# Kernel optimization log

Hardware: AMD Instinct MI355X
Metric: run time of the kernel (lower is better)

The kernel has to match this reference:

```python
import jax, jax.numpy as jnp
import numpy as np

N, E, D_IN, D_OUT = 50000, 800000, 128, 128
LN_EPS = 1e-5


def setup_inputs() -> dict:
    key = jax.random.key(0)
    ks = jax.random.split(key, 7)
    x = jax.random.normal(ks[0], (N, D_IN), dtype=jnp.float32)
    adj = jax.random.randint(ks[1], (2, E), 0, N, dtype=jnp.int32)  # edge_index
    scale = 1.0 / np.sqrt(D_IN)
    W_gcn = jax.random.normal(ks[2], (D_IN, D_OUT), dtype=jnp.float32) * scale
    b_gcn = jax.random.normal(ks[3], (D_OUT,), dtype=jnp.float32) * 0.02
    W_lin = jax.random.normal(ks[4], (D_IN, D_OUT), dtype=jnp.float32) * scale
    ln_w = jnp.ones((D_OUT,), dtype=jnp.float32)
    ln_b = jnp.zeros((D_OUT,), dtype=jnp.float32)
    return {"adj": adj, "x": x, "W_gcn": W_gcn, "b_gcn": b_gcn,
            "W_lin": W_lin, "ln_w": ln_w, "ln_b": ln_b}


def _gcn_conv(x, edge_index, W, b):
    """PyG GCNConv: add self-loops, symmetric D^-1/2 (A+I) D^-1/2 normalization."""
    n = x.shape[0]
    loop = jnp.arange(n, dtype=edge_index.dtype)
    src = jnp.concatenate([edge_index[0], loop])  # message sources (x_j)
    dst = jnp.concatenate([edge_index[1], loop])  # aggregation targets
    ones = jnp.ones(src.shape[0], dtype=x.dtype)
    deg = jax.ops.segment_sum(ones, dst, num_segments=n)
    dinv = jnp.where(deg > 0, jax.lax.rsqrt(deg), 0.0)
    norm = dinv[src] * dinv[dst]                   # [E+N]
    h = x @ W                                      # [N, D_OUT] project first (PyG order)
    msg = h[src] * norm[:, None]                   # gather + scale
    agg = jax.ops.segment_sum(msg, dst, num_segments=n)
    return agg + b


def _layer_norm(y, w, b):
    mu = jnp.mean(y, axis=-1, keepdims=True)
    var = jnp.mean(jnp.square(y - mu), axis=-1, keepdims=True)
    return (y - mu) * jax.lax.rsqrt(var + LN_EPS) * w + b


def reference(adj, x, W_gcn, b_gcn, W_lin, ln_w, ln_b):
    x1 = _gcn_conv(x, adj, W_gcn, b_gcn)
    x2 = x @ W_lin                                  # bias=False linear
    return _layer_norm(x1 + x2 + 1e-6, ln_w, ln_b)
```

## Files before the change

kernel.cpp:

```cpp
#include <hip/hip_runtime.h>
#include <hip/hip_bf16.h>

#define NN 50000
#define EE 800000
#define DD 128
#define NB 196

typedef __attribute__((ext_vector_type(8))) short bf16x8;
typedef __attribute__((ext_vector_type(4))) float f32x4;

static __device__ __forceinline__ unsigned short f2bf(float f) {
  union { float f; unsigned u; } v; v.f = f;
  unsigned r = v.u + 0x7FFFu + ((v.u >> 16) & 1u);
  return (unsigned short)(r >> 16);
}
static __device__ __forceinline__ float bf2f(unsigned short h) {
  union { unsigned u; float f; } v; v.u = ((unsigned)h) << 16;
  return v.f;
}

__global__ __launch_bounds__(256) void k_p0(const int* __restrict__ dst,
                                            int* __restrict__ bucketCnt,
                                            const float* __restrict__ Wg,
                                            const float* __restrict__ Wl,
                                            unsigned short* __restrict__ Wt) {
  int b = blockIdx.x, t = threadIdx.x;
  if (b < NB) {
    __shared__ int cnt[NB];
    for (int i = t; i < NB; i += 256) cnt[i] = 0;
    __syncthreads();
    int e0 = b * 4096;
    for (int i = t; i < 4096; i += 256) {
      int e = e0 + i;
      if (e < EE) atomicAdd(&cnt[dst[e] >> 8], 1);
    }
    __syncthreads();
    for (int i = t; i < NB; i += 256)
      if (cnt[i]) atomicAdd(&bucketCnt[i], cnt[i]);
  } else {
    for (int i = (b - NB) * 256 + t; i < DD * 256; i += 32 * 256) {
      int n = i >> 8, k = i & 255;
      float v = (k < 128) ? Wg[k * DD + n] : Wl[(k - 128) * DD + n];
      Wt[i] = f2bf(v);
    }
  }
}

__global__ __launch_bounds__(256) void k_pscan(const int* __restrict__ bucketCnt,
                                               int* __restrict__ bucketStart,
                                               int* __restrict__ cursor) {
  __shared__ int s[256];
  int t = threadIdx.x;
  int v = (t < NB) ? bucketCnt[t] : 0;
  s[t] = v;
  for (int off = 1; off < 256; off <<= 1) {
    __syncthreads();
    int tmp = (t >= off) ? s[t - off] : 0;
    __syncthreads();
    if (t >= off) s[t] += tmp;
  }
  __syncthreads();
  if (t < NB) {
    int excl = s[t] - v;
    bucketStart[t] = excl;
    cursor[t] = excl;
  }
}

__global__ __launch_bounds__(256) void k_p1(const int* __restrict__ src,
                                            const int* __restrict__ dst,
                                            int* __restrict__ cursor,
                                            unsigned int* __restrict__ pairs) {
  __shared__ unsigned int stage[4096];
  __shared__ int cnt[NB], base[NB], cur[NB];
  int t = threadIdx.x;
  int e0 = blockIdx.x * 4096;
  for (int i = t; i < NB; i += 256) { cnt[i] = 0; cur[i] = 0; }
  __syncthreads();
  for (int i = t; i < 4096; i += 256) {
    int e = e0 + i;
    unsigned int p = 0xFFFFFFFFu;
    if (e < EE) {
      int d = dst[e];
      int s = src[e];
      int bk = d >> 8;
      p = (unsigned int)s | ((unsigned int)(d & 255) << 16) | ((unsigned int)bk << 24);
      atomicAdd(&cnt[bk], 1);
    }
    stage[i] = p;
  }
  __syncthreads();
  for (int i = t; i < NB; i += 256)
    base[i] = cnt[i] ? atomicAdd(&cursor[i], cnt[i]) : 0;
  __syncthreads();
  for (int i = t; i < 4096; i += 256) {
    unsigned int p = stage[i];
    if (p != 0xFFFFFFFFu) {
      int bk = p >> 24;
      int ofs = atomicAdd(&cur[bk], 1);
      pairs[base[bk] + ofs] = p;
    }
  }
}

__global__ __launch_bounds__(256) void k_p2(
    const unsigned int* __restrict__ pairs, const int* __restrict__ bucketStart,
    const int* __restrict__ bucketCnt, const float4* __restrict__ x4,
    int* __restrict__ deg, float* __restrict__ dinv, int* __restrict__ rowStart,
    int* __restrict__ srcList, ushort4* __restrict__ xs4,
    ushort4* __restrict__ axc4) {
  int b = blockIdx.x, t = threadIdx.x;
  __shared__ int ldeg[256], lscan[256], lcur[256];
  __shared__ float ldinv[256];
  int n0 = b << 8;
  int nloc = NN - n0; if (nloc > 256) nloc = 256;
  int start = bucketStart[b], cnt = bucketCnt[b];
  ldeg[t] = 0;
  __syncthreads();
  for (int i = t; i < cnt; i += 256)
    atomicAdd(&ldeg[(pairs[start + i] >> 16) & 255], 1);
  __syncthreads();
  int dg = ldeg[t];
  lscan[t] = dg;
  for (int off = 1; off < 256; off <<= 1) {
    __syncthreads();
    int tmp = (t >= off) ? lscan[t - off] : 0;
    __syncthreads();
    if (t >= off) lscan[t] += tmp;
  }
  __syncthreads();
  int rs = start + lscan[t] - dg;
  lcur[t] = rs;
  float di = rsqrtf((float)(dg + 1));
  ldinv[t] = di;
  if (t < nloc) {
    deg[n0 + t] = dg;
    dinv[n0 + t] = di;
    rowStart[n0 + t] = rs;
  }
  __syncthreads();
  for (int i = t; i < cnt; i += 256) {
    unsigned int p = pairs[start + i];
    int pos = atomicAdd(&lcur[(p >> 16) & 255], 1);
    srcList[pos] = (int)(p & 0xFFFFu);
  }
  for (int i = t; i < nloc * 32; i += 256) {
    int r = i >> 5, c4 = i & 31;
    float4 v = x4[(size_t)(n0 + r) * 32 + c4];
    float d = ldinv[r];
    ushort4 s, rw;
    s.x = f2bf(v.x * d); s.y = f2bf(v.y * d);
    s.z = f2bf(v.z * d); s.w = f2bf(v.w * d);
    rw.x = f2bf(v.x); rw.y = f2bf(v.y); rw.z = f2bf(v.z); rw.w = f2bf(v.w);
    xs4[(size_t)(n0 + r) * 32 + c4] = s;
    axc4[(size_t)(n0 + r) * 64 + 32 + c4] = rw;
  }
}

__global__ __launch_bounds__(256) void k_agg(
    const unsigned short* __restrict__ xs, const float* __restrict__ dinv,
    const int* __restrict__ rowStart, const int* __restrict__ deg,
    const int* __restrict__ srcList, unsigned short* __restrict__ axc) {
  int t = threadIdx.x;
  int w = t >> 6, lane = t & 63;
  int node = blockIdx.x * 4 + w;
  if (node >= NN) return;
  int g = lane >> 4, r = lane & 15;
  int c0 = r * 8;
  float acc[8];
#pragma unroll
  for (int i = 0; i < 8; i++) acc[i] = 0.f;
  if (g == 0) {
    bf16x8 v = *(const bf16x8*)(xs + (size_t)node * DD + c0);
#pragma unroll
    for (int i = 0; i < 8; i++) acc[i] = bf2f((unsigned short)v[i]);
  }
  int start = rowStart[node], cnt = deg[node];
  int j0 = 2 * g, j1 = 2 * g + 1;
  int s0 = (j0 < cnt) ? srcList[start + j0] : -1;
  int s1 = (j1 < cnt) ? srcList[start + j1] : -1;
  for (int base = 0; base < cnt; base += 8) {
    int n0 = base + 8 + 2 * g, n1 = n0 + 1;
    int t0 = (n0 < cnt) ? srcList[start + n0] : -1;
    int t1 = (n1 < cnt) ? srcList[start + n1] : -1;
    if (s0 >= 0) {
      bf16x8 v = *(const bf16x8*)(xs + (size_t)s0 * DD + c0);
#pragma unroll
      for (int i = 0; i < 8; i++) acc[i] += bf2f((unsigned short)v[i]);
    }
    if (s1 >= 0) {
      bf16x8 v = *(const bf16x8*)(xs + (size_t)s1 * DD + c0);
#pragma unroll
      for (int i = 0; i < 8; i++) acc[i] += bf2f((unsigned short)v[i]);
    }
    s0 = t0; s1 = t1;
  }
#pragma unroll
  for (int i = 0; i < 8; i++) {
    acc[i] += __shfl_xor(acc[i], 16);
    acc[i] += __shfl_xor(acc[i], 32);
  }
  if (g == 0) {
    float di = dinv[node];
    bf16x8 o;
#pragma unroll
    for (int i = 0; i < 8; i++) o[i] = (short)f2bf(acc[i] * di);
    *(bf16x8*)(axc + (size_t)node * 256 + c0) = o;
  }
}

__global__ __launch_bounds__(256) void k_mm_ln(
    const unsigned short* __restrict__ axc, const unsigned short* __restrict__ Wt,
    const float* __restrict__ bgcn, const float* __restrict__ lnw,
    const float* __restrict__ lnb, float* __restrict__ out) {
  int t = threadIdx.x;
  int w = t >> 6, lane = t & 63;
  int quad = lane >> 4, r = lane & 15;
  int m0 = (blockIdx.x * 4 + w) * 16;
  f32x4 zero = {0.f, 0.f, 0.f, 0.f};
  f32x4 acc[8];
#pragma unroll
  for (int i = 0; i < 8; i++) acc[i] = zero;
  int rowA = m0 + r;
  if (rowA > NN - 1) rowA = NN - 1;
  const unsigned short* arow = axc + (size_t)rowA * 256 + quad * 8;
#pragma unroll
  for (int ks = 0; ks < 8; ks++) {
    bf16x8 a = *(const bf16x8*)(arow + ks * 32);
#pragma unroll
    for (int nt = 0; nt < 8; nt++) {
      bf16x8 b = *(const bf16x8*)(Wt + (size_t)(nt * 16 + r) * 256 + ks * 32 + quad * 8);
      acc[nt] = __builtin_amdgcn_mfma_f32_16x16x32_bf16(a, b, acc[nt], 0, 0, 0);
    }
  }
  float bg[8], lw[8], lb[8];
#pragma unroll
  for (int nt = 0; nt < 8; nt++) {
    int col = nt * 16 + r;
    bg[nt] = bgcn[col] + 1e-6f;
    lw[nt] = lnw[col];
    lb[nt] = lnb[col];
  }
#pragma unroll
  for (int reg = 0; reg < 4; reg++) {
    float y[8];
    float s1 = 0.f, s2 = 0.f;
#pragma unroll
    for (int nt = 0; nt < 8; nt++) {
      y[nt] = acc[nt][reg] + bg[nt];
      s1 += y[nt];
      s2 += y[nt] * y[nt];
    }
#pragma unroll
    for (int off = 1; off < 16; off <<= 1) {
      s1 += __shfl_xor(s1, off);
      s2 += __shfl_xor(s2, off);
    }
    float mu = s1 * (1.0f / 128.0f);
    float var = s2 * (1.0f / 128.0f) - mu * mu;
    float inv = rsqrtf(var + 1e-5f);
    int row = m0 + quad * 4 + reg;
    if (row < NN) {
#pragma unroll
      for (int nt = 0; nt < 8; nt++) {
        out[(size_t)row * DD + nt * 16 + r] = (y[nt] - mu) * inv * lw[nt] + lb[nt];
      }
    }
  }
}

extern "C" void kernel_launch(void* const* d_in, const int* in_sizes, int n_in,
                              void* d_out, int out_size, void* d_ws, size_t ws_size,
                              hipStream_t stream) {
  const int* adj = (const int*)d_in[0];
  const float* x = (const float*)d_in[1];
  const float* Wg = (const float*)d_in[2];
  const float* bg = (const float*)d_in[3];
  const float* Wl = (const float*)d_in[4];
  const float* lw = (const float*)d_in[5];
  const float* lb = (const float*)d_in[6];
  const int* srcp = adj;
  const int* dstp = adj + EE;
  float* out = (float*)d_out;

  char* ws = (char*)d_ws;
  size_t off = 0;
  auto alloc = [&](size_t bytes) -> void* {
    void* p = ws + off;
    off += (bytes + 255) & ~(size_t)255;
    return p;
  };
  int* bucketCnt = (int*)alloc(NB * 4);
  int* bucketStart = (int*)alloc(NB * 4);
  int* cursor = (int*)alloc(NB * 4);
  unsigned int* pairs = (unsigned int*)alloc((size_t)EE * 4);
  int* deg = (int*)alloc((size_t)NN * 4);
  float* dinv = (float*)alloc((size_t)NN * 4);
  int* rowStart = (int*)alloc((size_t)NN * 4);
  int* srcList = (int*)alloc((size_t)EE * 4);
  unsigned short* xs = (unsigned short*)alloc((size_t)NN * DD * 2);
  unsigned short* axc = (unsigned short*)alloc((size_t)NN * 256 * 2);
  unsigned short* Wt = (unsigned short*)alloc((size_t)DD * 256 * 2);
  (void)ws_size; (void)in_sizes; (void)n_in; (void)out_size;

  hipMemsetAsync(bucketCnt, 0, NB * 4, stream);
  k_p0<<<NB + 32, 256, 0, stream>>>(dstp, bucketCnt, Wg, Wl, Wt);
  k_pscan<<<1, 256, 0, stream>>>(bucketCnt, bucketStart, cursor);
  k_p1<<<NB, 256, 0, stream>>>(srcp, dstp, cursor, pairs);
  k_p2<<<NB, 256, 0, stream>>>(pairs, bucketStart, bucketCnt, (const float4*)x,
                               deg, dinv, rowStart, srcList, (ushort4*)xs,
                               (ushort4*)axc);
  k_agg<<<(NN + 3) / 4, 256, 0, stream>>>(xs, dinv, rowStart, deg, srcList, axc);
  k_mm_ln<<<(NN + 63) / 64, 256, 0, stream>>>(axc, Wt, bg, lw, lb, out);
}
```

Measured before the change: 208.4 us.

## Fuse aggregation, projection and LayerNorm into one per-bucket LDS-atomic kernel

Result: slower. 826.1 us (+296.4%).

```diff
diff --git a/kernel.cpp b/kernel.cpp
--- a/kernel.cpp
+++ b/kernel.cpp
@@ -4,7 +4,9 @@
 #define NN 50000
 #define EE 800000
 #define DD 128
-#define NB 196
+#define NB 391
+#define EBLK 4096
+#define NEB 196
 
 typedef __attribute__((ext_vector_type(8))) short bf16x8;
 typedef __attribute__((ext_vector_type(4))) float f32x4;
@@ -19,41 +21,53 @@
   return v.f;
 }
 
-__global__ __launch_bounds__(256) void k_p0(const int* __restrict__ dst,
-                                            int* __restrict__ bucketCnt,
-                                            const float* __restrict__ Wg,
-                                            const float* __restrict__ Wl,
-                                            unsigned short* __restrict__ Wt) {
+__global__ __launch_bounds__(256) void k_p0(
+    const int* __restrict__ dst, int* __restrict__ bucketCnt,
+    const float* __restrict__ Wg, const float* __restrict__ Wl,
+    unsigned short* __restrict__ Wt, const float4* __restrict__ x4,
+    ushort4* __restrict__ xb4) {
   int b = blockIdx.x, t = threadIdx.x;
-  if (b < NB) {
+  if (b < NEB) {
     __shared__ int cnt[NB];
     for (int i = t; i < NB; i += 256) cnt[i] = 0;
     __syncthreads();
-    int e0 = b * 4096;
-    for (int i = t; i < 4096; i += 256) {
+    int e0 = b * EBLK;
+    for (int i = t; i < EBLK; i += 256) {
       int e = e0 + i;
-      if (e < EE) atomicAdd(&cnt[dst[e] >> 8], 1);
+      if (e < EE) atomicAdd(&cnt[dst[e] >> 7], 1);
     }
     __syncthreads();
     for (int i = t; i < NB; i += 256)
       if (cnt[i]) atomicAdd(&bucketCnt[i], cnt[i]);
-  } else {
-    for (int i = (b - NB) * 256 + t; i < DD * 256; i += 32 * 256) {
+  } else if (b < NEB + 32) {
+    for (int i = (b - NEB) * 256 + t; i < DD * 256; i += 32 * 256) {
       int n = i >> 8, k = i & 255;
       float v = (k < 128) ? Wg[k * DD + n] : Wl[(k - 128) * DD + n];
       Wt[i] = f2bf(v);
     }
-  }
-}
-
-__global__ __launch_bounds__(256) void k_pscan(const int* __restrict__ bucketCnt,
+  } else {
+    int base = (b - NEB - 32) * 1024;
+#pragma unroll
+    for (int k = 0; k < 4; k++) {
+      int i = base + t + k * 256;
+      if (i < NN * 32) {
+        float4 v = x4[i];
+        ushort4 o;
+        o.x = f2bf(v.x); o.y = f2bf(v.y); o.z = f2bf(v.z); o.w = f2bf(v.w);
+        xb4[i] = o;
+      }
+    }
+  }
+}
+
+__global__ __launch_bounds__(512) void k_pscan(const int* __restrict__ bucketCnt,
                                                int* __restrict__ bucketStart,
                                                int* __restrict__ cursor) {
-  __shared__ int s[256];
+  __shared__ int s[512];
   int t = threadIdx.x;
   int v = (t < NB) ? bucketCnt[t] : 0;
   s[t] = v;
-  for (int off = 1; off < 256; off <<= 1) {
+  for (int off = 1; off < 512; off <<= 1) {
     __syncthreads();
     int tmp = (t >= off) ? s[t - off] : 0;
     __syncthreads();
@@ -61,9 +75,8 @@
   }
   __syncthreads();
   if (t < NB) {
-    int excl = s[t] - v;
-    bucketStart[t] = excl;
-    cursor[t] = excl;
+    bucketStart[t] = s[t] - v;
+    cursor[t] = s[t] - v;
   }
 }
 
@@ -71,166 +84,143 @@
                                             const int* __restrict__ dst,
                                             int* __restrict__ cursor,
                                             unsigned int* __restrict__ pairs) {
-  __shared__ unsigned int stage[4096];
-  __shared__ int cnt[NB], base[NB], cur[NB];
+  __shared__ unsigned int stage[EBLK];
+  __shared__ int cnt[NB], base_[NB], cur[NB];
   int t = threadIdx.x;
-  int e0 = blockIdx.x * 4096;
+  int e0 = blockIdx.x * EBLK;
   for (int i = t; i < NB; i += 256) { cnt[i] = 0; cur[i] = 0; }
   __syncthreads();
-  for (int i = t; i < 4096; i += 256) {
+  for (int i = t; i < EBLK; i += 256) {
     int e = e0 + i;
     unsigned int p = 0xFFFFFFFFu;
     if (e < EE) {
-      int d = dst[e];
-      int s = src[e];
-      int bk = d >> 8;
-      p = (unsigned int)s | ((unsigned int)(d & 255) << 16) | ((unsigned int)bk << 24);
+      int d = dst[e], s = src[e];
+      int bk = d >> 7;
+      p = (unsigned int)s | ((unsigned int)(d & 127) << 16) | ((unsigned int)bk << 23);
       atomicAdd(&cnt[bk], 1);
     }
     stage[i] = p;
   }
   __syncthreads();
   for (int i = t; i < NB; i += 256)
-    base[i] = cnt[i] ? atomicAdd(&cursor[i], cnt[i]) : 0;
-  __syncthreads();
-  for (int i = t; i < 4096; i += 256) {
+    base_[i] = cnt[i] ? atomicAdd(&cursor[i], cnt[i]) : 0;
+  __syncthreads();
+  for (int i = t; i < EBLK; i += 256) {
     unsigned int p = stage[i];
     if (p != 0xFFFFFFFFu) {
-      int bk = p >> 24;
+      int bk = p >> 23;
       int ofs = atomicAdd(&cur[bk], 1);
-      pairs[base[bk] + ofs] = p;
-    }
-  }
-}
-
-__global__ __launch_bounds__(256) void k_p2(
+      pairs[base_[bk] + ofs] = p;
+    }
+  }
+}
+
+__global__ __launch_bounds__(256) void k_pdeg(const unsigned int* __restrict__ pairs,
+                                              const int* __restrict__ bucketStart,
+                                              const int* __restrict__ bucketCnt,
+                                              float* __restrict__ dinv) {
+  __shared__ int ldeg[128];
+  int b = blockIdx.x, t = threadIdx.x;
+  if (t < 128) ldeg[t] = 0;
+  __syncthreads();
+  int start = bucketStart[b], cnt = bucketCnt[b];
+  for (int i = t; i < cnt; i += 256)
+    atomicAdd(&ldeg[(pairs[start + i] >> 16) & 127], 1);
+  __syncthreads();
+  int n0 = b << 7;
+  if (t < 128 && n0 + t < NN)
+    dinv[n0 + t] = rsqrtf((float)(ldeg[t] + 1));
+}
+
+__global__ __launch_bounds__(512, 4) void k_mega(
     const unsigned int* __restrict__ pairs, const int* __restrict__ bucketStart,
-    const int* __restrict__ bucketCnt, const float4* __restrict__ x4,
-    int* __restrict__ deg, float* __restrict__ dinv, int* __restrict__ rowStart,
-    int* __restrict__ srcList, ushort4* __restrict__ xs4,
-    ushort4* __restrict__ axc4) {
-  int b = blockIdx.x, t = threadIdx.x;
-  __shared__ int ldeg[256], lscan[256], lcur[256];
-  __shared__ float ldinv[256];
-  int n0 = b << 8;
-  int nloc = NN - n0; if (nloc > 256) nloc = 256;
-  int start = bucketStart[b], cnt = bucketCnt[b];
-  ldeg[t] = 0;
-  __syncthreads();
-  for (int i = t; i < cnt; i += 256)
-    atomicAdd(&ldeg[(pairs[start + i] >> 16) & 255], 1);
-  __syncthreads();
-  int dg = ldeg[t];
-  lscan[t] = dg;
-  for (int off = 1; off < 256; off <<= 1) {
-    __syncthreads();
-    int tmp = (t >= off) ? lscan[t - off] : 0;
-    __syncthreads();
-    if (t >= off) lscan[t] += tmp;
-  }
-  __syncthreads();
-  int rs = start + lscan[t] - dg;
-  lcur[t] = rs;
-  float di = rsqrtf((float)(dg + 1));
-  ldinv[t] = di;
-  if (t < nloc) {
-    deg[n0 + t] = dg;
-    dinv[n0 + t] = di;
-    rowStart[n0 + t] = rs;
-  }
-  __syncthreads();
-  for (int i = t; i < cnt; i += 256) {
-    unsigned int p = pairs[start + i];
-    int pos = atomicAdd(&lcur[(p >> 16) & 255], 1);
-    srcList[pos] = (int)(p & 0xFFFFu);
-  }
-  for (int i = t; i < nloc * 32; i += 256) {
-    int r = i >> 5, c4 = i & 31;
-    float4 v = x4[(size_t)(n0 + r) * 32 + c4];
-    float d = ldinv[r];
-    ushort4 s, rw;
-    s.x = f2bf(v.x * d); s.y = f2bf(v.y * d);
-    s.z = f2bf(v.z * d); s.w = f2bf(v.w * d);
-    rw.x = f2bf(v.x); rw.y = f2bf(v.y); rw.z = f2bf(v.z); rw.w = f2bf(v.w);
-    xs4[(size_t)(n0 + r) * 32 + c4] = s;
-    axc4[(size_t)(n0 + r) * 64 + 32 + c4] = rw;
-  }
-}
-
-__global__ __launch_bounds__(256) void k_agg(
-    const unsigned short* __restrict__ xs, const float* __restrict__ dinv,
-    const int* __restrict__ rowStart, const int* __restrict__ deg,
-    const int* __restrict__ srcList, unsigned short* __restrict__ axc) {
-  int t = threadIdx.x;
-  int w = t >> 6, lane = t & 63;
-  int node = blockIdx.x * 4 + w;
-  if (node >= NN) return;
-  int g = lane >> 4, r = lane & 15;
-  int c0 = r * 8;
-  float acc[8];
-#pragma unroll
-  for (int i = 0; i < 8; i++) acc[i] = 0.f;
-  if (g == 0) {
-    bf16x8 v = *(const bf16x8*)(xs + (size_t)node * DD + c0);
-#pragma unroll
-    for (int i = 0; i < 8; i++) acc[i] = bf2f((unsigned short)v[i]);
-  }
-  int start = rowStart[node], cnt = deg[node];
-  int j0 = 2 * g, j1 = 2 * g + 1;
-  int s0 = (j0 < cnt) ? srcList[start + j0] : -1;
-  int s1 = (j1 < cnt) ? srcList[start + j1] : -1;
-  for (int base = 0; base < cnt; base += 8) {
-    int n0 = base + 8 + 2 * g, n1 = n0 + 1;
-    int t0 = (n0 < cnt) ? srcList[start + n0] : -1;
-    int t1 = (n1 < cnt) ? srcList[start + n1] : -1;
-    if (s0 >= 0) {
-      bf16x8 v = *(const bf16x8*)(xs + (size_t)s0 * DD + c0);
-#pragma unroll
-      for (int i = 0; i < 8; i++) acc[i] += bf2f((unsigned short)v[i]);
-    }
-    if (s1 >= 0) {
-      bf16x8 v = *(const bf16x8*)(xs + (size_t)s1 * DD + c0);
-#pragma unroll
-      for (int i = 0; i < 8; i++) acc[i] += bf2f((unsigned short)v[i]);
-    }
-    s0 = t0; s1 = t1;
-  }
-#pragma unroll
-  for (int i = 0; i < 8; i++) {
-    acc[i] += __shfl_xor(acc[i], 16);
-    acc[i] += __shfl_xor(acc[i], 32);
-  }
-  if (g == 0) {
-    float di = dinv[node];
-    bf16x8 o;
-#pragma unroll
-    for (int i = 0; i < 8; i++) o[i] = (short)f2bf(acc[i] * di);
-    *(bf16x8*)(axc + (size_t)node * 256 + c0) = o;
-  }
-}
-
-__global__ __launch_bounds__(256) void k_mm_ln(
-    const unsigned short* __restrict__ axc, const unsigned short* __restrict__ Wt,
+    const int* __restrict__ bucketCnt, const unsigned short* __restrict__ xb,
+    const float* __restrict__ dinv, const unsigned short* __restrict__ Wt,
     const float* __restrict__ bgcn, const float* __restrict__ lnw,
     const float* __restrict__ lnb, float* __restrict__ out) {
-  int t = threadIdx.x;
+  __shared__ float acc[128 * 128];
+  int b = blockIdx.x, t = threadIdx.x;
+  int n0 = b << 7;
+  {
+    int rr = t >> 2;
+    int c0 = (t & 3) * 32;
+    int row = n0 + rr; if (row > NN - 1) row = NN - 1;
+    float di = dinv[row];
+    const ushort4* xr = (const ushort4*)(xb + (size_t)row * DD + c0);
+#pragma unroll
+    for (int q = 0; q < 8; q++) {
+      ushort4 u = xr[q];
+      int c = c0 + q * 4;
+      float4 wv;
+      wv.x = bf2f(u.x) * di; wv.y = bf2f(u.y) * di;
+      wv.z = bf2f(u.z) * di; wv.w = bf2f(u.w) * di;
+      *(float4*)&acc[rr * 128 + ((c + 4 * rr) & 127)] = wv;
+    }
+  }
+  __syncthreads();
+  {
+    int start = bucketStart[b], cnt = bucketCnt[b];
+    int g = t >> 4, r = t & 15;
+    int i = g;
+    unsigned int pA = (i < cnt) ? pairs[start + i] : 0;
+    unsigned int pB = (i + 32 < cnt) ? pairs[start + i + 32] : 0;
+    while (i < cnt) {
+      int inext = i + 64;
+      unsigned int nA = (inext < cnt) ? pairs[start + inext] : 0;
+      unsigned int nB = (inext + 32 < cnt) ? pairs[start + inext + 32] : 0;
+      int sA = pA & 0xFFFF, dA = (pA >> 16) & 127;
+      int sB = pB & 0xFFFF, dB = (pB >> 16) & 127;
+      bf16x8 vA = *(const bf16x8*)(xb + (size_t)sA * DD + r * 8);
+      float diA = dinv[sA];
+      bf16x8 vB = *(const bf16x8*)(xb + (size_t)sB * DD + r * 8);
+      float diB = dinv[sB];
+      int baseA = dA * 128, rotA = 8 * r + 4 * dA;
+#pragma unroll
+      for (int j = 0; j < 8; j++) {
+        int jj = (j + r) & 7;
+        atomicAdd(&acc[baseA + ((rotA + jj) & 127)],
+                  bf2f((unsigned short)vA[jj]) * diA);
+      }
+      if (i + 32 < cnt) {
+        int baseB = dB * 128, rotB = 8 * r + 4 * dB;
+#pragma unroll
+        for (int j = 0; j < 8; j++) {
+          int jj = (j + r) & 7;
+          atomicAdd(&acc[baseB + ((rotB + jj) & 127)],
+                    bf2f((unsigned short)vB[jj]) * diB);
+        }
+      }
+      i = inext; pA = nA; pB = nB;
+    }
+  }
+  __syncthreads();
   int w = t >> 6, lane = t & 63;
   int quad = lane >> 4, r = lane & 15;
-  int m0 = (blockIdx.x * 4 + w) * 16;
+  int mloc = w * 16 + r;
+  int rowA = n0 + mloc; if (rowA > NN - 1) rowA = NN - 1;
+  float diRow = dinv[rowA];
   f32x4 zero = {0.f, 0.f, 0.f, 0.f};
-  f32x4 acc[8];
-#pragma unroll
-  for (int i = 0; i < 8; i++) acc[i] = zero;
-  int rowA = m0 + r;
-  if (rowA > NN - 1) rowA = NN - 1;
-  const unsigned short* arow = axc + (size_t)rowA * 256 + quad * 8;
+  f32x4 macc[8];
+#pragma unroll
+  for (int idx = 0; idx < 8; idx++) macc[idx] = zero;
 #pragma unroll
   for (int ks = 0; ks < 8; ks++) {
-    bf16x8 a = *(const bf16x8*)(arow + ks * 32);
+    bf16x8 a;
+    if (ks < 4) {
+      int c = ks * 32 + quad * 8;
+      float4 q0 = *(const float4*)&acc[mloc * 128 + ((c + 4 * mloc) & 127)];
+      float4 q1 = *(const float4*)&acc[mloc * 128 + ((c + 4 + 4 * mloc) & 127)];
+      a[0] = (short)f2bf(q0.x * diRow); a[1] = (short)f2bf(q0.y * diRow);
+      a[2] = (short)f2bf(q0.z * diRow); a[3] = (short)f2bf(q0.w * diRow);
+      a[4] = (short)f2bf(q1.x * diRow); a[5] = (short)f2bf(q1.y * diRow);
+      a[6] = (short)f2bf(q1.z * diRow); a[7] = (short)f2bf(q1.w * diRow);
+    } else {
+      a = *(const bf16x8*)(xb + (size_t)rowA * DD + (ks - 4) * 32 + quad * 8);
+    }
 #pragma unroll
     for (int nt = 0; nt < 8; nt++) {
-      bf16x8 b = *(const bf16x8*)(Wt + (size_t)(nt * 16 + r) * 256 + ks * 32 + quad * 8);
-      acc[nt] = __builtin_amdgcn_mfma_f32_16x16x32_bf16(a, b, acc[nt], 0, 0, 0);
+      bf16x8 bb = *(const bf16x8*)(Wt + (size_t)(nt * 16 + r) * 256 + ks * 32 + quad * 8);
+      macc[nt] = __builtin_amdgcn_mfma_f32_16x16x32_bf16(a, bb, macc[nt], 0, 0, 0);
     }
   }
   float bg[8], lw[8], lb[8];
@@ -247,7 +237,7 @@
     float s1 = 0.f, s2 = 0.f;
 #pragma unroll
     for (int nt = 0; nt < 8; nt++) {
-      y[nt] = acc[nt][reg] + bg[nt];
+      y[nt] = macc[nt][reg] + bg[nt];
       s1 += y[nt];
       s2 += y[nt] * y[nt];
     }
@@ -259,7 +249,7 @@
     float mu = s1 * (1.0f / 128.0f);
     float var = s2 * (1.0f / 128.0f) - mu * mu;
     float inv = rsqrtf(var + 1e-5f);
-    int row = m0 + quad * 4 + reg;
+    int row = n0 + w * 16 + quad * 4 + reg;
     if (row < NN) {
 #pragma unroll
       for (int nt = 0; nt < 8; nt++) {
@@ -294,22 +284,17 @@
   int* bucketStart = (int*)alloc(NB * 4);
   int* cursor = (int*)alloc(NB * 4);
   unsigned int* pairs = (unsigned int*)alloc((size_t)EE * 4);
-  int* deg = (int*)alloc((size_t)NN * 4);
   float* dinv = (float*)alloc((size_t)NN * 4);
-  int* rowStart = (int*)alloc((size_t)NN * 4);
-  int* srcList = (int*)alloc((size_t)EE * 4);
-  unsigned short* xs = (unsigned short*)alloc((size_t)NN * DD * 2);
-  unsigned short* axc = (unsigned short*)alloc((size_t)NN * 256 * 2);
+  unsigned short* xb = (unsigned short*)alloc((size_t)NN * DD * 2);
   unsigned short* Wt = (unsigned short*)alloc((size_t)DD * 256 * 2);
   (void)ws_size; (void)in_sizes; (void)n_in; (void)out_size;
 
   hipMemsetAsync(bucketCnt, 0, NB * 4, stream);
-  k_p0<<<NB + 32, 256, 0, stream>>>(dstp, bucketCnt, Wg, Wl, Wt);
-  k_pscan<<<1, 256, 0, stream>>>(bucketCnt, bucketStart, cursor);
-  k_p1<<<NB, 256, 0, stream>>>(srcp, dstp, cursor, pairs);
-  k_p2<<<NB, 256, 0, stream>>>(pairs, bucketStart, bucketCnt, (const float4*)x,
-                               deg, dinv, rowStart, srcList, (ushort4*)xs,
-                               (ushort4*)axc);
-  k_agg<<<(NN + 3) / 4, 256, 0, stream>>>(xs, dinv, rowStart, deg, srcList, axc);
-  k_mm_ln<<<(NN + 63) / 64, 256, 0, stream>>>(axc, Wt, bg, lw, lb, out);
-}
+  k_p0<<<NEB + 32 + 1568, 256, 0, stream>>>(dstp, bucketCnt, Wg, Wl, Wt,
+                                            (const float4*)x, (ushort4*)xb);
+  k_pscan<<<1, 512, 0, stream>>>(bucketCnt, bucketStart, cursor);
+  k_p1<<<NEB, 256, 0, stream>>>(srcp, dstp, cursor, pairs);
+  k_pdeg<<<NB, 256, 0, stream>>>(pairs, bucketStart, bucketCnt, dinv);
+  k_mega<<<NB, 512, 0, stream>>>(pairs, bucketStart, bucketCnt, xb, dinv, Wt,
+                                 bg, lw, lb, out);
+}
```
